# Kernel tuning notes

Measured on AMD Instinct MI355X. Metric: run time of the kernel, lower is better.

## Reference

```python
import jax, jax.numpy as jnp
import numpy as np

S, C, HF, WF = 6, 64, 44, 80          # cameras, feat channels, feat H, feat W
H_IMG, W_IMG = 352.0, 640.0           # full image size (opt.height/opt.width)
Z, Y, X = 16, 100, 100                # voxel grid (opt.voxels_size)
XMIN, XMAX = -40.0, 40.0
YMIN, YMAX = -40.0, 40.0
ZMIN, ZMAX = -1.0, 5.4
EPS = 1e-6


def setup_inputs() -> dict:
    key = jax.random.key(0)
    features = jax.random.normal(jax.random.fold_in(key, 0), (S, C, HF, WF), dtype=jnp.float32)
    # intrinsics at full image resolution
    K = np.eye(4, dtype=np.float32)
    K[0, 0] = 500.0; K[1, 1] = 500.0
    K[0, 2] = W_IMG / 2.0; K[1, 2] = H_IMG / 2.0
    pix_T_cams = np.tile(K[None], (S, 1, 1))
    # 6-camera surround rig: cam0_T_camX rigid transforms (columns = camera axes in ref frame)
    mats = []
    for i in range(S):
        th = 2.0 * np.pi * i / S
        c, s = np.cos(th), np.sin(th)
        T = np.eye(4, dtype=np.float32)
        T[:3, 0] = [-s, c, 0.0]          # camera x (right)
        T[:3, 1] = [0.0, 0.0, -1.0]      # camera y (down)
        T[:3, 2] = [c, s, 0.0]           # camera z (forward)
        T[:3, 3] = [0.5 * c, 0.5 * s, 1.5]
        mats.append(T)
    cam0_T_camXs = np.stack(mats).astype(np.float32)
    return {"features": features,
            "pix_T_cams": jnp.asarray(pix_T_cams),
            "cam0_T_camXs": jnp.asarray(cam0_T_camXs)}


def _safe_inverse(T):
    # rigid 4x4 inverse: [R t] -> [R^T, -R^T t]
    R = T[:, :3, :3]
    t = T[:, :3, 3]
    Rt = jnp.swapaxes(R, 1, 2)
    tt = -jnp.einsum('sij,sj->si', Rt, t)
    inv = jnp.zeros_like(T)
    inv = inv.at[:, :3, :3].set(Rt).at[:, :3, 3].set(tt).at[:, 3, 3].set(1.0)
    return inv


def _voxel_centers():
    # ref-frame coordinates of voxel centers, flattened [Z*Y*X, 3] with x fastest
    vx = (XMAX - XMIN) / X
    vy = (YMAX - YMIN) / Y
    vz = (ZMAX - ZMIN) / Z
    xs = XMIN + vx * (jnp.arange(X, dtype=jnp.float32) + 0.5)
    ys = YMIN + vy * (jnp.arange(Y, dtype=jnp.float32) + 0.5)
    zs = ZMIN + vz * (jnp.arange(Z, dtype=jnp.float32) + 0.5)
    zz, yy, xx = jnp.meshgrid(zs, ys, xs, indexing='ij')
    return jnp.stack([xx, yy, zz], axis=-1).reshape(-1, 3)


def _bilinear(img, x, y):
    # img: [C,H,W]; x,y: [N] pixel coords; zero padding outside
    Hh, Ww = img.shape[-2], img.shape[-1]
    x0 = jnp.floor(x)
    y0 = jnp.floor(y)
    wx1 = x - x0
    wy1 = y - y0

    def corner(xi, yi, w):
        valid = (xi >= 0) & (xi < Ww) & (yi >= 0) & (yi < Hh)
        xc = jnp.clip(xi, 0, Ww - 1).astype(jnp.int32)
        yc = jnp.clip(yi, 0, Hh - 1).astype(jnp.int32)
        return img[:, yc, xc] * (w * valid)[None, :]

    return (corner(x0, y0, (1 - wx1) * (1 - wy1))
            + corner(x0 + 1, y0, wx1 * (1 - wy1))
            + corner(x0, y0 + 1, (1 - wx1) * wy1)
            + corner(x0 + 1, y0 + 1, wx1 * wy1))  # [C,N]


def reference(features, pix_T_cams, cam0_T_camXs):
    camXs_T_cam0 = _safe_inverse(cam0_T_camXs)
    sx, sy = WF / W_IMG, HF / H_IMG
    scale = jnp.diag(jnp.array([sx, sy, 1.0, 1.0], jnp.float32))
    featpix_T_cams = jnp.einsum('ij,sjk->sik', scale, pix_T_cams)
    pix_T_cam0 = jnp.einsum('sij,sjk->sik', featpix_T_cams, camXs_T_cam0)

    xyz0 = _voxel_centers()                                  # [N,3]
    xyz1 = jnp.concatenate([xyz0, jnp.ones((xyz0.shape[0], 1), jnp.float32)], -1)
    xyz_pix = jnp.einsum('sij,nj->sni', pix_T_cam0, xyz1)    # [S,N,4]
    z_cam = jnp.einsum('sj,nj->sn', camXs_T_cam0[:, 2, :], xyz1)  # camX-frame depth

    denom = jnp.maximum(xyz_pix[..., 2], 1e-6)
    x_pix = xyz_pix[..., 0] / denom
    y_pix = xyz_pix[..., 1] / denom
    valid = ((x_pix > -0.5) & (x_pix < WF - 0.5)
             & (y_pix > -0.5) & (y_pix < HF - 0.5)
             & (z_cam > 0.0))

    # grid_sample(align_corners=False) with norm 2*(p/W)-1 samples at pixel p-0.5
    samp = jax.vmap(_bilinear)(features, x_pix - 0.5, y_pix - 0.5)  # [S,C,N]
    feat_mems = samp * valid[:, None, :].astype(samp.dtype)
    feat_mems = feat_mems.reshape(S, C, Z, Y, X)[None]              # [1,S,C,Z,Y,X]

    mask = (jnp.abs(feat_mems) > 0).astype(feat_mems.dtype)
    feat_mem = (feat_mems * mask).sum(1) / (mask.sum(1) + EPS)      # masked mean over cams
    return jnp.transpose(feat_mem, (0, 1, 4, 3, 2))                 # [1,C,X,Y,Z]
```

## Files before the change

### kernel.cpp

```cpp
#include <hip/hip_runtime.h>

#define NS 6
#define NC 64
#define HF 44
#define WF 80
#define HW (HF * WF)
#define NZ 16
#define NY 100
#define NX 100
#define XYZ (NX * NY * NZ)

__global__ __launch_bounds__(256) void transpose_feat(
        const float* __restrict__ in, float* __restrict__ outT) {
    __shared__ float tile[64 * 65];
    int b = blockIdx.x;
    int s = b / 55;
    int hw0 = (b % 55) * 64;
    int t = threadIdx.x;
#pragma unroll
    for (int i = 0; i < 16; ++i) {
        int e = t + i * 256;
        int c = e >> 6, w = e & 63;
        tile[c * 65 + w] = in[((size_t)(s * NC + c)) * HW + hw0 + w];
    }
    __syncthreads();
#pragma unroll
    for (int i = 0; i < 16; ++i) {
        int e = t + i * 256;
        int hwl = e >> 6, c = e & 63;
        outT[((size_t)s * HW + hw0 + hwl) * NC + c] = tile[c * 65 + hwl];
    }
}

template <bool TRANS>
__global__ __launch_bounds__(256) void volpool(
        const float* __restrict__ feat,
        const float* __restrict__ pix,
        const float* __restrict__ c0TX,
        float* __restrict__ out) {
    __shared__ float  mlds[NS * 16];
    __shared__ float4 wts[96];
    __shared__ int4   offs[96];
    __shared__ int    vflags[96];
    __shared__ float  ostage[NC * 17];

    int t = threadIdx.x;
    int b = blockIdx.x;
    int x = b % NX, y = b / NX;

    if (t < NS) {
        const float* T = c0TX + t * 16;
        float inv[4][4];
        for (int i = 0; i < 3; ++i) {
            for (int j = 0; j < 3; ++j) inv[i][j] = T[j * 4 + i];
            inv[i][3] = -(T[0 * 4 + i] * T[0 * 4 + 3] +
                          T[1 * 4 + i] * T[1 * 4 + 3] +
                          T[2 * 4 + i] * T[2 * 4 + 3]);
        }
        inv[3][0] = 0.f; inv[3][1] = 0.f; inv[3][2] = 0.f; inv[3][3] = 1.f;
        const float sx = (float)WF / 640.0f;
        const float sy = (float)HF / 352.0f;
        const float* K = pix + t * 16;
        float fp[3][4];
        for (int j = 0; j < 4; ++j) {
            fp[0][j] = sx * K[0 * 4 + j];
            fp[1][j] = sy * K[1 * 4 + j];
            fp[2][j] = K[2 * 4 + j];
        }
        float* M = mlds + t * 16;
        for (int i = 0; i < 3; ++i)
            for (int j = 0; j < 4; ++j) {
                float acc = 0.f;
                for (int k = 0; k < 4; ++k) acc += fp[i][k] * inv[k][j];
                M[i * 4 + j] = acc;
            }
        for (int j = 0; j < 4; ++j) M[12 + j] = inv[2][j];
    }
    __syncthreads();

    if (t < 96) {
        int s = t % NS, z = t / NS;
        const float* M = mlds + s * 16;
        float xw = -40.0f + 0.8f * ((float)x + 0.5f);
        float yw = -40.0f + 0.8f * ((float)y + 0.5f);
        float zw = -1.0f + 0.4f * ((float)z + 0.5f);
        float px = M[0] * xw + M[1] * yw + M[2]  * zw + M[3];
        float py = M[4] * xw + M[5] * yw + M[6]  * zw + M[7];
        float pz = M[8] * xw + M[9] * yw + M[10] * zw + M[11];
        float zc = M[12] * xw + M[13] * yw + M[14] * zw + M[15];
        float denom = fmaxf(pz, 1e-6f);
        float xp = px / denom, yp = py / denom;
        bool valid = (xp > -0.5f) & (xp < (float)WF - 0.5f) &
                     (yp > -0.5f) & (yp < (float)HF - 0.5f) & (zc > 0.0f);
        vflags[t] = valid ? 1 : 0;
        if (valid) {
            float xs = xp - 0.5f, ys = yp - 0.5f;
            float x0f = floorf(xs), y0f = floorf(ys);
            float wx1 = xs - x0f, wy1 = ys - y0f;
            float wx0 = 1.f - wx1, wy0 = 1.f - wy1;
            int x0 = (int)x0f, y0 = (int)y0f;
            int x1 = x0 + 1, y1 = y0 + 1;
            bool bx0 = (x0 >= 0) & (x0 < WF);
            bool bx1 = (x1 >= 0) & (x1 < WF);
            bool by0 = (y0 >= 0) & (y0 < HF);
            bool by1 = (y1 >= 0) & (y1 < HF);
            int x0c = min(max(x0, 0), WF - 1);
            int x1c = min(max(x1, 0), WF - 1);
            int y0c = min(max(y0, 0), HF - 1);
            int y1c = min(max(y1, 0), HF - 1);
            float4 w;
            w.x = wx0 * wy0 * (float)(bx0 & by0);
            w.y = wx1 * wy0 * (float)(bx1 & by0);
            w.z = wx0 * wy1 * (float)(bx0 & by1);
            w.w = wx1 * wy1 * (float)(bx1 & by1);
            int p00 = y0c * WF + x0c, p10 = y0c * WF + x1c;
            int p01 = y1c * WF + x0c, p11 = y1c * WF + x1c;
            int4 o;
            if (TRANS) {
                o.x = (s * HW + p00) * NC;
                o.y = (s * HW + p10) * NC;
                o.z = (s * HW + p01) * NC;
                o.w = (s * HW + p11) * NC;
            } else {
                o.x = s * NC * HW + p00;
                o.y = s * NC * HW + p10;
                o.z = s * NC * HW + p01;
                o.w = s * NC * HW + p11;
            }
            wts[t] = w;
            offs[t] = o;
        }
    }
    __syncthreads();

    int cg = t & 15, z = t >> 4;
    float4 sum = make_float4(0.f, 0.f, 0.f, 0.f);
    float4 cnt = make_float4(0.f, 0.f, 0.f, 0.f);
    for (int s = 0; s < NS; ++s) {
        int idx = z * NS + s;
        if (!vflags[idx]) continue;
        float4 w = wts[idx];
        int4 o = offs[idx];
        float4 f00, f10, f01, f11;
        if (TRANS) {
            int ch4 = cg << 2;
            f00 = *(const float4*)(feat + o.x + ch4);
            f10 = *(const float4*)(feat + o.y + ch4);
            f01 = *(const float4*)(feat + o.z + ch4);
            f11 = *(const float4*)(feat + o.w + ch4);
        } else {
            int c0 = cg << 2;
            f00.x = feat[o.x + (c0 + 0) * HW]; f00.y = feat[o.x + (c0 + 1) * HW];
            f00.z = feat[o.x + (c0 + 2) * HW]; f00.w = feat[o.x + (c0 + 3) * HW];
            f10.x = feat[o.y + (c0 + 0) * HW]; f10.y = feat[o.y + (c0 + 1) * HW];
            f10.z = feat[o.y + (c0 + 2) * HW]; f10.w = feat[o.y + (c0 + 3) * HW];
            f01.x = feat[o.z + (c0 + 0) * HW]; f01.y = feat[o.z + (c0 + 1) * HW];
            f01.z = feat[o.z + (c0 + 2) * HW]; f01.w = feat[o.z + (c0 + 3) * HW];
            f11.x = feat[o.w + (c0 + 0) * HW]; f11.y = feat[o.w + (c0 + 1) * HW];
            f11.z = feat[o.w + (c0 + 2) * HW]; f11.w = feat[o.w + (c0 + 3) * HW];
        }
        float vx = w.x * f00.x + w.y * f10.x + w.z * f01.x + w.w * f11.x;
        float vy = w.x * f00.y + w.y * f10.y + w.z * f01.y + w.w * f11.y;
        float vz = w.x * f00.z + w.y * f10.z + w.z * f01.z + w.w * f11.z;
        float vw = w.x * f00.w + w.y * f10.w + w.z * f01.w + w.w * f11.w;
        sum.x += vx; cnt.x += (vx != 0.0f) ? 1.0f : 0.0f;
        sum.y += vy; cnt.y += (vy != 0.0f) ? 1.0f : 0.0f;
        sum.z += vz; cnt.z += (vz != 0.0f) ? 1.0f : 0.0f;
        sum.w += vw; cnt.w += (vw != 0.0f) ? 1.0f : 0.0f;
    }
    int c0 = cg << 2;
    ostage[(c0 + 0) * 17 + z] = sum.x / (cnt.x + 1e-6f);
    ostage[(c0 + 1) * 17 + z] = sum.y / (cnt.y + 1e-6f);
    ostage[(c0 + 2) * 17 + z] = sum.z / (cnt.z + 1e-6f);
    ostage[(c0 + 3) * 17 + z] = sum.w / (cnt.w + 1e-6f);
    __syncthreads();

    int c = t >> 2, zq = t & 3;
    float4 v4;
    v4.x = ostage[c * 17 + zq * 4 + 0];
    v4.y = ostage[c * 17 + zq * 4 + 1];
    v4.z = ostage[c * 17 + zq * 4 + 2];
    v4.w = ostage[c * 17 + zq * 4 + 3];
    float* o = out + (size_t)c * XYZ + ((size_t)x * NY + y) * NZ + zq * 4;
    *(float4*)o = v4;
}

extern "C" void kernel_launch(void* const* d_in, const int* in_sizes, int n_in,
                              void* d_out, int out_size, void* d_ws, size_t ws_size,
                              hipStream_t stream) {
    const float* features = (const float*)d_in[0];
    const float* pix      = (const float*)d_in[1];
    const float* c0TX     = (const float*)d_in[2];
    float* out   = (float*)d_out;
    float* featT = (float*)d_ws;
    size_t need = sizeof(float) * (size_t)NS * HW * NC;

    if (ws_size >= need) {
        hipLaunchKernelGGL(transpose_feat, dim3(NS * 55), dim3(256), 0, stream,
                           features, featT);
        hipLaunchKernelGGL((volpool<true>), dim3(NX * NY), dim3(256), 0, stream,
                           featT, pix, c0TX, out);
    } else {
        hipLaunchKernelGGL((volpool<false>), dim3(NX * NY), dim3(256), 0, stream,
                           features, pix, c0TX, out);
    }
}
```

Measured before the change: 87.59 us.

## Process four x-columns per block, precompute camera matrices, compact valid cameras

```diff
diff --git a/kernel.cpp b/kernel.cpp
--- a/kernel.cpp
+++ b/kernel.cpp
@@ -9,79 +9,107 @@
 #define NY 100
 #define NX 100
 #define XYZ (NX * NY * NZ)
+#define COLS 4
+#define NPAR (COLS * NZ * NS)
+
+typedef float v4f __attribute__((ext_vector_type(4)));
+
+__device__ void compute_mats(int s, const float* __restrict__ pix,
+                             const float* __restrict__ c0TX,
+                             float* __restrict__ mats) {
+    const float* T = c0TX + s * 16;
+    float inv[4][4];
+    for (int i = 0; i < 3; ++i) {
+        for (int j = 0; j < 3; ++j) inv[i][j] = T[j * 4 + i];
+        inv[i][3] = -(T[0 * 4 + i] * T[0 * 4 + 3] +
+                      T[1 * 4 + i] * T[1 * 4 + 3] +
+                      T[2 * 4 + i] * T[2 * 4 + 3]);
+    }
+    inv[3][0] = 0.f; inv[3][1] = 0.f; inv[3][2] = 0.f; inv[3][3] = 1.f;
+    const float sx = (float)WF / 640.0f;
+    const float sy = (float)HF / 352.0f;
+    const float* K = pix + s * 16;
+    float fp[3][4];
+    for (int j = 0; j < 4; ++j) {
+        fp[0][j] = sx * K[0 * 4 + j];
+        fp[1][j] = sy * K[1 * 4 + j];
+        fp[2][j] = K[2 * 4 + j];
+    }
+    float* M = mats + s * 16;
+    for (int i = 0; i < 3; ++i)
+        for (int j = 0; j < 4; ++j) {
+            float acc = 0.f;
+            for (int k = 0; k < 4; ++k) acc += fp[i][k] * inv[k][j];
+            M[i * 4 + j] = acc;
+        }
+    for (int j = 0; j < 4; ++j) M[12 + j] = inv[2][j];
+}
 
 __global__ __launch_bounds__(256) void transpose_feat(
-        const float* __restrict__ in, float* __restrict__ outT) {
+        const float* __restrict__ in, float* __restrict__ outT,
+        const float* __restrict__ pix, const float* __restrict__ c0TX,
+        float* __restrict__ mats) {
     __shared__ float tile[64 * 65];
     int b = blockIdx.x;
+    int t = threadIdx.x;
+    if (b == 0 && t < NS) compute_mats(t, pix, c0TX, mats);
     int s = b / 55;
     int hw0 = (b % 55) * 64;
-    int t = threadIdx.x;
-#pragma unroll
-    for (int i = 0; i < 16; ++i) {
+#pragma unroll
+    for (int i = 0; i < 4; ++i) {
         int e = t + i * 256;
-        int c = e >> 6, w = e & 63;
-        tile[c * 65 + w] = in[((size_t)(s * NC + c)) * HW + hw0 + w];
-    }
-    __syncthreads();
-#pragma unroll
-    for (int i = 0; i < 16; ++i) {
+        int c = e >> 4, wg = e & 15;
+        float4 f = *(const float4*)(in + ((size_t)(s * NC + c)) * HW + hw0 + wg * 4);
+        tile[c * 65 + wg * 4 + 0] = f.x;
+        tile[c * 65 + wg * 4 + 1] = f.y;
+        tile[c * 65 + wg * 4 + 2] = f.z;
+        tile[c * 65 + wg * 4 + 3] = f.w;
+    }
+    __syncthreads();
+#pragma unroll
+    for (int i = 0; i < 4; ++i) {
         int e = t + i * 256;
-        int hwl = e >> 6, c = e & 63;
-        outT[((size_t)s * HW + hw0 + hwl) * NC + c] = tile[c * 65 + hwl];
-    }
+        int hwl = e >> 4, cg = e & 15;
+        float4 f;
+        f.x = tile[(cg * 4 + 0) * 65 + hwl];
+        f.y = tile[(cg * 4 + 1) * 65 + hwl];
+        f.z = tile[(cg * 4 + 2) * 65 + hwl];
+        f.w = tile[(cg * 4 + 3) * 65 + hwl];
+        *(float4*)(outT + ((size_t)s * HW + hw0 + hwl) * NC + cg * 4) = f;
+    }
+}
+
+__global__ void setup_mats(const float* __restrict__ pix,
+                           const float* __restrict__ c0TX,
+                           float* __restrict__ mats) {
+    int s = threadIdx.x;
+    if (s < NS) compute_mats(s, pix, c0TX, mats);
 }
 
 template <bool TRANS>
 __global__ __launch_bounds__(256) void volpool(
         const float* __restrict__ feat,
-        const float* __restrict__ pix,
-        const float* __restrict__ c0TX,
+        const float* __restrict__ mats,
         float* __restrict__ out) {
-    __shared__ float  mlds[NS * 16];
-    __shared__ float4 wts[96];
-    __shared__ int4   offs[96];
-    __shared__ int    vflags[96];
-    __shared__ float  ostage[NC * 17];
+    __shared__ float4 wts[NPAR];
+    __shared__ int4   offs[NPAR];
+    __shared__ int    vflags[NPAR];
+    __shared__ int    vidx[COLS][NZ][NS];
+    __shared__ int    nvalid[COLS][NZ];
+    __shared__ float  ostage[COLS][NC * 17];
 
     int t = threadIdx.x;
     int b = blockIdx.x;
-    int x = b % NX, y = b / NX;
-
-    if (t < NS) {
-        const float* T = c0TX + t * 16;
-        float inv[4][4];
-        for (int i = 0; i < 3; ++i) {
-            for (int j = 0; j < 3; ++j) inv[i][j] = T[j * 4 + i];
-            inv[i][3] = -(T[0 * 4 + i] * T[0 * 4 + 3] +
-                          T[1 * 4 + i] * T[1 * 4 + 3] +
-                          T[2 * 4 + i] * T[2 * 4 + 3]);
-        }
-        inv[3][0] = 0.f; inv[3][1] = 0.f; inv[3][2] = 0.f; inv[3][3] = 1.f;
-        const float sx = (float)WF / 640.0f;
-        const float sy = (float)HF / 352.0f;
-        const float* K = pix + t * 16;
-        float fp[3][4];
-        for (int j = 0; j < 4; ++j) {
-            fp[0][j] = sx * K[0 * 4 + j];
-            fp[1][j] = sy * K[1 * 4 + j];
-            fp[2][j] = K[2 * 4 + j];
-        }
-        float* M = mlds + t * 16;
-        for (int i = 0; i < 3; ++i)
-            for (int j = 0; j < 4; ++j) {
-                float acc = 0.f;
-                for (int k = 0; k < 4; ++k) acc += fp[i][k] * inv[k][j];
-                M[i * 4 + j] = acc;
-            }
-        for (int j = 0; j < 4; ++j) M[12 + j] = inv[2][j];
-    }
-    __syncthreads();
-
-    if (t < 96) {
-        int s = t % NS, z = t / NS;
-        const float* M = mlds + s * 16;
-        float xw = -40.0f + 0.8f * ((float)x + 0.5f);
+    int x0 = (b % (NX / COLS)) * COLS;
+    int y  = b / (NX / COLS);
+
+    for (int p = t; p < NPAR; p += 256) {
+        int col  = p / 96;
+        int rest = p - col * 96;
+        int s = rest % NS;
+        int z = rest / NS;
+        const float* M = mats + s * 16;
+        float xw = -40.0f + 0.8f * ((float)(x0 + col) + 0.5f);
         float yw = -40.0f + 0.8f * ((float)y + 0.5f);
         float zw = -1.0f + 0.4f * ((float)z + 0.5f);
         float px = M[0] * xw + M[1] * yw + M[2]  * zw + M[3];
@@ -92,22 +120,22 @@
         float xp = px / denom, yp = py / denom;
         bool valid = (xp > -0.5f) & (xp < (float)WF - 0.5f) &
                      (yp > -0.5f) & (yp < (float)HF - 0.5f) & (zc > 0.0f);
-        vflags[t] = valid ? 1 : 0;
+        vflags[p] = valid ? 1 : 0;
         if (valid) {
             float xs = xp - 0.5f, ys = yp - 0.5f;
             float x0f = floorf(xs), y0f = floorf(ys);
             float wx1 = xs - x0f, wy1 = ys - y0f;
             float wx0 = 1.f - wx1, wy0 = 1.f - wy1;
-            int x0 = (int)x0f, y0 = (int)y0f;
-            int x1 = x0 + 1, y1 = y0 + 1;
-            bool bx0 = (x0 >= 0) & (x0 < WF);
-            bool bx1 = (x1 >= 0) & (x1 < WF);
-            bool by0 = (y0 >= 0) & (y0 < HF);
-            bool by1 = (y1 >= 0) & (y1 < HF);
-            int x0c = min(max(x0, 0), WF - 1);
-            int x1c = min(max(x1, 0), WF - 1);
-            int y0c = min(max(y0, 0), HF - 1);
-            int y1c = min(max(y1, 0), HF - 1);
+            int xi0 = (int)x0f, yi0 = (int)y0f;
+            int xi1 = xi0 + 1, yi1 = yi0 + 1;
+            bool bx0 = (xi0 >= 0) & (xi0 < WF);
+            bool bx1 = (xi1 >= 0) & (xi1 < WF);
+            bool by0 = (yi0 >= 0) & (yi0 < HF);
+            bool by1 = (yi1 >= 0) & (yi1 < HF);
+            int x0c = min(max(xi0, 0), WF - 1);
+            int x1c = min(max(xi1, 0), WF - 1);
+            int y0c = min(max(yi0, 0), HF - 1);
+            int y1c = min(max(yi1, 0), HF - 1);
             float4 w;
             w.x = wx0 * wy0 * (float)(bx0 & by0);
             w.y = wx1 * wy0 * (float)(bx1 & by0);
@@ -127,62 +155,78 @@
                 o.z = s * NC * HW + p01;
                 o.w = s * NC * HW + p11;
             }
-            wts[t] = w;
-            offs[t] = o;
+            wts[p] = w;
+            offs[p] = o;
         }
     }
     __syncthreads();
 
+    if (t < COLS * NZ) {
+        int col = t >> 4, z = t & 15;
+        int base = col * 96 + z * NS;
+        int n = 0;
+        for (int s = 0; s < NS; ++s)
+            if (vflags[base + s]) vidx[col][z][n++] = base + s;
+        nvalid[col][z] = n;
+    }
+    __syncthreads();
+
     int cg = t & 15, z = t >> 4;
-    float4 sum = make_float4(0.f, 0.f, 0.f, 0.f);
-    float4 cnt = make_float4(0.f, 0.f, 0.f, 0.f);
-    for (int s = 0; s < NS; ++s) {
-        int idx = z * NS + s;
-        if (!vflags[idx]) continue;
-        float4 w = wts[idx];
-        int4 o = offs[idx];
-        float4 f00, f10, f01, f11;
-        if (TRANS) {
-            int ch4 = cg << 2;
-            f00 = *(const float4*)(feat + o.x + ch4);
-            f10 = *(const float4*)(feat + o.y + ch4);
-            f01 = *(const float4*)(feat + o.z + ch4);
-            f11 = *(const float4*)(feat + o.w + ch4);
-        } else {
-            int c0 = cg << 2;
-            f00.x = feat[o.x + (c0 + 0) * HW]; f00.y = feat[o.x + (c0 + 1) * HW];
-            f00.z = feat[o.x + (c0 + 2) * HW]; f00.w = feat[o.x + (c0 + 3) * HW];
-            f10.x = feat[o.y + (c0 + 0) * HW]; f10.y = feat[o.y + (c0 + 1) * HW];
-            f10.z = feat[o.y + (c0 + 2) * HW]; f10.w = feat[o.y + (c0 + 3) * HW];
-            f01.x = feat[o.z + (c0 + 0) * HW]; f01.y = feat[o.z + (c0 + 1) * HW];
-            f01.z = feat[o.z + (c0 + 2) * HW]; f01.w = feat[o.z + (c0 + 3) * HW];
-            f11.x = feat[o.w + (c0 + 0) * HW]; f11.y = feat[o.w + (c0 + 1) * HW];
-            f11.z = feat[o.w + (c0 + 2) * HW]; f11.w = feat[o.w + (c0 + 3) * HW];
+    int ch4 = cg << 2;
+#pragma unroll
+    for (int col = 0; col < COLS; ++col) {
+        float4 sum = make_float4(0.f, 0.f, 0.f, 0.f);
+        float4 cnt = make_float4(0.f, 0.f, 0.f, 0.f);
+        int nv = nvalid[col][z];
+        for (int j = 0; j < nv; ++j) {
+            int idx = vidx[col][z][j];
+            float4 w = wts[idx];
+            int4 o = offs[idx];
+            float4 f00, f10, f01, f11;
+            if (TRANS) {
+                f00 = *(const float4*)(feat + o.x + ch4);
+                f10 = *(const float4*)(feat + o.y + ch4);
+                f01 = *(const float4*)(feat + o.z + ch4);
+                f11 = *(const float4*)(feat + o.w + ch4);
+            } else {
+                f00.x = feat[o.x + (ch4 + 0) * HW]; f00.y = feat[o.x + (ch4 + 1) * HW];
+                f00.z = feat[o.x + (ch4 + 2) * HW]; f00.w = feat[o.x + (ch4 + 3) * HW];
+                f10.x = feat[o.y + (ch4 + 0) * HW]; f10.y = feat[o.y + (ch4 + 1) * HW];
+                f10.z = feat[o.y + (ch4 + 2) * HW]; f10.w = feat[o.y + (ch4 + 3) * HW];
+                f01.x = feat[o.z + (ch4 + 0) * HW]; f01.y = feat[o.z + (ch4 + 1) * HW];
+                f01.z = feat[o.z + (ch4 + 2) * HW]; f01.w = feat[o.z + (ch4 + 3) * HW];
+                f11.x = feat[o.w + (ch4 + 0) * HW]; f11.y = feat[o.w + (ch4 + 1) * HW];
+                f11.z = feat[o.w + (ch4 + 2) * HW]; f11.w = feat[o.w + (ch4 + 3) * HW];
+            }
+            float vx = w.x * f00.x + w.y * f10.x + w.z * f01.x + w.w * f11.x;
+            float vy = w.x * f00.y + w.y * f10.y + w.z * f01.y + w.w * f11.y;
+            float vz = w.x * f00.z + w.y * f10.z + w.z * f01.z + w.w * f11.z;
+            float vw = w.x * f00.w + w.y * f10.w + w.z * f01.w + w.w * f11.w;
+            sum.x += vx; cnt.x += (vx != 0.0f) ? 1.0f : 0.0f;
+            sum.y += vy; cnt.y += (vy != 0.0f) ? 1.0f : 0.0f;
+            sum.z += vz; cnt.z += (vz != 0.0f) ? 1.0f : 0.0f;
+            sum.w += vw; cnt.w += (vw != 0.0f) ? 1.0f : 0.0f;
         }
-        float vx = w.x * f00.x + w.y * f10.x + w.z * f01.x + w.w * f11.x;
-        float vy = w.x * f00.y + w.y * f10.y + w.z * f01.y + w.w * f11.y;
-        float vz = w.x * f00.z + w.y * f10.z + w.z * f01.z + w.w * f11.z;
-        float vw = w.x * f00.w + w.y * f10.w + w.z * f01.w + w.w * f11.w;
-        sum.x += vx; cnt.x += (vx != 0.0f) ? 1.0f : 0.0f;
-        sum.y += vy; cnt.y += (vy != 0.0f) ? 1.0f : 0.0f;
-        sum.z += vz; cnt.z += (vz != 0.0f) ? 1.0f : 0.0f;
-        sum.w += vw; cnt.w += (vw != 0.0f) ? 1.0f : 0.0f;
-    }
-    int c0 = cg << 2;
-    ostage[(c0 + 0) * 17 + z] = sum.x / (cnt.x + 1e-6f);
-    ostage[(c0 + 1) * 17 + z] = sum.y / (cnt.y + 1e-6f);
-    ostage[(c0 + 2) * 17 + z] = sum.z / (cnt.z + 1e-6f);
-    ostage[(c0 + 3) * 17 + z] = sum.w / (cnt.w + 1e-6f);
+        float* os = &ostage[col][0];
+        os[(ch4 + 0) * 17 + z] = sum.x / (cnt.x + 1e-6f);
+        os[(ch4 + 1) * 17 + z] = sum.y / (cnt.y + 1e-6f);
+        os[(ch4 + 2) * 17 + z] = sum.z / (cnt.z + 1e-6f);
+        os[(ch4 + 3) * 17 + z] = sum.w / (cnt.w + 1e-6f);
+    }
     __syncthreads();
 
     int c = t >> 2, zq = t & 3;
-    float4 v4;
-    v4.x = ostage[c * 17 + zq * 4 + 0];
-    v4.y = ostage[c * 17 + zq * 4 + 1];
-    v4.z = ostage[c * 17 + zq * 4 + 2];
-    v4.w = ostage[c * 17 + zq * 4 + 3];
-    float* o = out + (size_t)c * XYZ + ((size_t)x * NY + y) * NZ + zq * 4;
-    *(float4*)o = v4;
+#pragma unroll
+    for (int col = 0; col < COLS; ++col) {
+        v4f v4;
+        v4.x = ostage[col][c * 17 + zq * 4 + 0];
+        v4.y = ostage[col][c * 17 + zq * 4 + 1];
+        v4.z = ostage[col][c * 17 + zq * 4 + 2];
+        v4.w = ostage[col][c * 17 + zq * 4 + 3];
+        float* o = out + (size_t)c * XYZ +
+                   ((size_t)(x0 + col) * NY + y) * NZ + zq * 4;
+        __builtin_nontemporal_store(v4, (v4f*)o);
+    }
 }
 
 extern "C" void kernel_launch(void* const* d_in, const int* in_sizes, int n_in,
@@ -192,16 +236,19 @@
     const float* pix      = (const float*)d_in[1];
     const float* c0TX     = (const float*)d_in[2];
     float* out   = (float*)d_out;
-    float* featT = (float*)d_ws;
-    size_t need = sizeof(float) * (size_t)NS * HW * NC;
+    float* mats  = (float*)d_ws;
+    float* featT = (float*)((char*)d_ws + 512);
+    size_t need = 512 + sizeof(float) * (size_t)NS * HW * NC;
 
     if (ws_size >= need) {
         hipLaunchKernelGGL(transpose_feat, dim3(NS * 55), dim3(256), 0, stream,
-                           features, featT);
-        hipLaunchKernelGGL((volpool<true>), dim3(NX * NY), dim3(256), 0, stream,
-                           featT, pix, c0TX, out);
+                           features, featT, pix, c0TX, mats);
+        hipLaunchKernelGGL((volpool<true>), dim3((NX / COLS) * NY), dim3(256),
+                           0, stream, featT, mats, out);
     } else {
-        hipLaunchKernelGGL((volpool<false>), dim3(NX * NY), dim3(256), 0, stream,
-                           features, pix, c0TX, out);
-    }
-}
+        hipLaunchKernelGGL(setup_mats, dim3(1), dim3(64), 0, stream,
+                           pix, c0TX, mats);
+        hipLaunchKernelGGL((volpool<false>), dim3((NX / COLS) * NY), dim3(256),
+                           0, stream, features, mats, out);
+    }
+}
```

Measured after the change: 89.16 us. About the same (+1.8%).
